# Kernel optimization log

Measured on AMD Instinct MI355X. Metric: run time of the kernel, lower is better.

## Reference

```python
import jax, jax.numpy as jnp
import numpy as np

NEG_INF = -1e9


def setup_inputs() -> dict:
    key = jax.random.key(0)
    ks = jax.random.split(key, 8)
    B, S, D = 8, 2048, 1024
    scale = 1.0 / np.sqrt(D)
    src = jax.random.normal(ks[0], (B, S, D), dtype=jnp.float32)
    pad_len = jax.random.randint(ks[1], (B,), 0, S // 10)
    pos = jnp.arange(S)[None, :]
    src_padding_mask = jnp.where(pos >= (S - pad_len)[:, None], NEG_INF, 0.0).astype(jnp.float32)[:, :, None]
    # causal (subsequent) additive mask [S,S]
    src_subsq_mask = jnp.where(jnp.triu(jnp.ones((S, S), dtype=bool), k=1), NEG_INF, 0.0).astype(jnp.float32)
    Wk = jax.random.normal(ks[2], (D, D), dtype=jnp.float32) * scale
    Wv = jax.random.normal(ks[3], (D, D), dtype=jnp.float32) * scale
    Wq = jax.random.normal(ks[4], (D, D), dtype=jnp.float32) * scale
    bk = jnp.zeros((D,), dtype=jnp.float32)
    bv = jnp.zeros((D,), dtype=jnp.float32)
    bq = jnp.zeros((D,), dtype=jnp.float32)
    return {"src": src, "src_padding_mask": src_padding_mask, "src_subsq_mask": src_subsq_mask,
            "Wk": Wk, "bk": bk, "Wv": Wv, "bv": bv, "Wq": Wq, "bq": bq}


def reference(src, src_padding_mask, src_subsq_mask, Wk, bk, Wv, bv, Wq, bq):
    d_model = src.shape[-1]
    # torch nn.Linear: x @ W.T + b
    keys = jnp.einsum('bsd,ed->bse', src, Wk) + bk
    values = jnp.einsum('bsd,ed->bse', src, Wv) + bv
    queries = jnp.einsum('bsd,ed->bse', src, Wq) + bq
    sqrt_d = jnp.asarray(d_model, src.dtype) ** 0.5
    att = jnp.einsum('bqd,bkd->bqk', queries, keys) / sqrt_d   # [B,S,S]
    att = att + jnp.swapaxes(src_padding_mask, 1, 2)           # [B,1,S] broadcast
    att = att + src_subsq_mask[None, :, :]                      # [1,S,S] broadcast
    att_softmax = jax.nn.softmax(att, axis=2)
    att_out = jnp.einsum('bqk,bkd->bqd', att_softmax, values)
    return att_out
```

## Files before the change

kernel.cpp:

```cpp
#include <hip/hip_runtime.h>
#include <cstdint>
#include <cstddef>

#define BATCH 8
#define SEQ   2048
#define DM    1024

typedef _Float16 half8 __attribute__((ext_vector_type(8)));
typedef _Float16 half4v __attribute__((ext_vector_type(4)));
typedef float floatx4 __attribute__((ext_vector_type(4)));
typedef float float4v __attribute__((ext_vector_type(4)));

#define GLOBAL_AS __attribute__((address_space(1)))
#define LDS_AS    __attribute__((address_space(3)))

__device__ __forceinline__ void gl_lds16(const _Float16* g, _Float16* l) {
    __builtin_amdgcn_global_load_lds((const GLOBAL_AS void*)g, (LDS_AS void*)l, 16, 0, 0);
}

__device__ __forceinline__ void gemm_bt_tile(
    const _Float16* __restrict__ A, const _Float16* __restrict__ B,
    int lda, int ldb, int kmax,
    _Float16* As, _Float16* Bs, floatx4 (&acc)[4][4])
{
    const int t = threadIdx.x;
    const int wave = t >> 6, lane = t & 63;
    const int l15 = lane & 15, kq = lane >> 4;
    const int wm = (wave >> 1) * 64, wn = (wave & 1) * 64;
    const int srow = wave * 8 + (lane >> 3);
    const int schunk = lane & 7;
    _Float16* AsW = As + wave * 512;
    _Float16* BsW = Bs + wave * 512;
    const int cslot = ((kq ^ (l15 & 7)) * 8);
    const int cslot1 = (((4 + kq) ^ (l15 & 7)) * 8);

    for (int k0 = 0; k0 < kmax; k0 += 64) {
        __syncthreads();
        #pragma unroll
        for (int i = 0; i < 4; i++) {
            const int r = srow + i * 32;
            const int gcol = (schunk ^ (r & 7)) * 8;
            gl_lds16(A + (size_t)r * lda + k0 + gcol, AsW + i * 2048);
            gl_lds16(B + (size_t)r * ldb + k0 + gcol, BsW + i * 2048);
        }
        __syncthreads();

        {
            half8 af[4], bfr[4];
            #pragma unroll
            for (int i = 0; i < 4; i++)
                af[i] = *(const half8*)&As[(wm + i * 16 + l15) * 64 + cslot];
            #pragma unroll
            for (int j = 0; j < 4; j++)
                bfr[j] = *(const half8*)&Bs[(wn + j * 16 + l15) * 64 + cslot];
            #pragma unroll
            for (int i = 0; i < 4; i++)
                #pragma unroll
                for (int j = 0; j < 4; j++)
                    acc[i][j] = __builtin_amdgcn_mfma_f32_16x16x32_f16(af[i], bfr[j], acc[i][j], 0, 0, 0);
        }
        {
            half8 af[4], bfr[4];
            #pragma unroll
            for (int i = 0; i < 4; i++)
                af[i] = *(const half8*)&As[(wm + i * 16 + l15) * 64 + cslot1];
            #pragma unroll
            for (int j = 0; j < 4; j++)
                bfr[j] = *(const half8*)&Bs[(wn + j * 16 + l15) * 64 + cslot1];
            #pragma unroll
            for (int i = 0; i < 4; i++)
                #pragma unroll
                for (int j = 0; j < 4; j++)
                    acc[i][j] = __builtin_amdgcn_mfma_f32_16x16x32_f16(af[i], bfr[j], acc[i][j], 0, 0, 0);
        }
    }
}

__global__ __launch_bounds__(256) void convert_inputs(
    const float* __restrict__ src,
    const float* __restrict__ Wk, const float* __restrict__ Wv, const float* __restrict__ Wq,
    _Float16* __restrict__ Xh, _Float16* __restrict__ Wh)
{
    const int gid = blockIdx.x * 256 + threadIdx.x;
    const int gs  = gridDim.x * 256;
    const int nX4 = BATCH * SEQ * DM / 4;
    const int nW4 = DM * DM / 4;
    const float4v* s4  = (const float4v*)src;
    const float4v* wk4 = (const float4v*)Wk;
    const float4v* wv4 = (const float4v*)Wv;
    const float4v* wq4 = (const float4v*)Wq;
    half4v* x4 = (half4v*)Xh;
    half4v* w4 = (half4v*)Wh;
    for (int i = gid; i < nX4; i += gs) {
        float4v v = s4[i];
        half4v h;
        #pragma unroll
        for (int e = 0; e < 4; e++) h[e] = (_Float16)v[e];
        x4[i] = h;
    }
    for (int i = gid; i < nW4; i += gs) {
        float4v a = wk4[i], b = wv4[i], c = wq4[i];
        half4v ha, hb, hc;
        #pragma unroll
        for (int e = 0; e < 4; e++) { ha[e] = (_Float16)a[e]; hb[e] = (_Float16)b[e]; hc[e] = (_Float16)c[e]; }
        w4[i]           = ha;
        w4[nW4 + i]     = hb;
        w4[2 * nW4 + i] = hc;
    }
}

__global__ __launch_bounds__(256) void qkv_gemm(
    const _Float16* __restrict__ Xh, const _Float16* __restrict__ Wh,
    const float* __restrict__ bk, const float* __restrict__ bv, const float* __restrict__ bq,
    _Float16* __restrict__ Kh, _Float16* __restrict__ Vt, _Float16* __restrict__ Qh)
{
    __shared__ __align__(16) _Float16 As[128 * 64];
    __shared__ __align__(16) _Float16 Bs[128 * 64];
    const int L = blockIdx.x;
    const int x = L & 7, s = L >> 3;
    const int z = s >> 7;
    const int r = s & 127;
    const int by = x * 16 + (r >> 3);
    const int bx = r & 7;

    const _Float16 *A, *B;
    if (z == 1) {
        A = Wh + (size_t)DM * DM + (size_t)bx * 128 * DM;
        B = Xh + (size_t)by * 128 * DM;
    } else {
        A = Xh + (size_t)by * 128 * DM;
        B = Wh + (z == 0 ? (size_t)0 : (size_t)2 * DM * DM) + (size_t)bx * 128 * DM;
    }
    floatx4 acc[4][4] = {};
    gemm_bt_tile(A, B, DM, DM, DM, As, Bs, acc);

    const int lane = threadIdx.x & 63, wave = threadIdx.x >> 6;
    const int l15 = lane & 15, kq = lane >> 4;
    const int wm = (wave >> 1) * 64, wn = (wave & 1) * 64;
    if (z == 1) {
        const int b = by >> 4, st = by & 15;
        #pragma unroll
        for (int i = 0; i < 4; i++)
            #pragma unroll
            for (int j = 0; j < 4; j++)
                #pragma unroll
                for (int rr = 0; rr < 4; rr++) {
                    int d = bx * 128 + wm + i * 16 + kq * 4 + rr;
                    int sIdx = st * 128 + wn + j * 16 + l15;
                    Vt[((size_t)b * DM + d) * SEQ + sIdx] = (_Float16)(acc[i][j][rr] + bv[d]);
                }
    } else {
        const float* bias = (z == 0) ? bk : bq;
        _Float16* outp    = (z == 0) ? Kh : Qh;
        #pragma unroll
        for (int i = 0; i < 4; i++)
            #pragma unroll
            for (int j = 0; j < 4; j++)
                #pragma unroll
                for (int rr = 0; rr < 4; rr++) {
                    int row = by * 128 + wm + i * 16 + kq * 4 + rr;
                    int col = bx * 128 + wn + j * 16 + l15;
                    outp[(size_t)row * DM + col] = (_Float16)(acc[i][j][rr] + bias[col]);
                }
    }
}

__global__ __launch_bounds__(256) void scores_gemm(
    const _Float16* __restrict__ Qh, const _Float16* __restrict__ Kh,
    const float* __restrict__ pad, _Float16* __restrict__ Sc)
{
    __shared__ __align__(16) _Float16 As[128 * 64];
    __shared__ __align__(16) _Float16 Bs[128 * 64];
    const int L = blockIdx.x;
    const int x = L & 7, s = L >> 3;
    const int b = s / 17, w = s % 17;
    int by, bx;
    if (w < 16 - x) { by = 15 - x; bx = w; }
    else            { by = x;      bx = w - (16 - x); }

    const _Float16* A = Qh + ((size_t)b * SEQ + by * 128) * DM;
    const _Float16* B = Kh + ((size_t)b * SEQ + bx * 128) * DM;
    floatx4 acc[4][4] = {};
    gemm_bt_tile(A, B, DM, DM, DM, As, Bs, acc);

    const int lane = threadIdx.x & 63, wave = threadIdx.x >> 6;
    const int l15 = lane & 15, kq = lane >> 4;
    const int wm = (wave >> 1) * 64, wn = (wave & 1) * 64;
    #pragma unroll
    for (int i = 0; i < 4; i++)
        #pragma unroll
        for (int j = 0; j < 4; j++)
            #pragma unroll
            for (int r = 0; r < 4; r++) {
                int row = by * 128 + wm + i * 16 + kq * 4 + r;
                int col = bx * 128 + wn + j * 16 + l15;
                Sc[((size_t)b * SEQ + row) * SEQ + col] =
                    (_Float16)(acc[i][j][r] * 0.03125f + pad[b * SEQ + col]);
            }
}

__global__ __launch_bounds__(256) void softmax_rows(_Float16* __restrict__ Sc)
{
    const int bid = blockIdx.x;
    const int b = bid >> 11, q = bid & (SEQ - 1);
    _Float16* row = Sc + ((size_t)b * SEQ + q) * SEQ;
    const int n = q + 1;
    const int kmaxr = ((q >> 7) + 1) << 7;
    const int t = threadIdx.x;
    const int c0 = t * 8;
    const bool active = (c0 < kmaxr);
    __shared__ float red[4];

    half8 v = {};
    if (active) v = *(const half8*)(row + c0);
    float f[8];
    float m = -3.0e38f;
    #pragma unroll
    for (int e = 0; e < 8; e++) {
        f[e] = (active && (c0 + e < n)) ? (float)v[e] : -3.0e38f;
        m = fmaxf(m, f[e]);
    }
    #pragma unroll
    for (int o = 32; o > 0; o >>= 1) m = fmaxf(m, __shfl_down(m, o));
    if ((t & 63) == 0) red[t >> 6] = m;
    __syncthreads();
    m = fmaxf(fmaxf(red[0], red[1]), fmaxf(red[2], red[3]));

    float ex[8], s = 0.f;
    #pragma unroll
    for (int e = 0; e < 8; e++) {
        ex[e] = (f[e] > -1.0e38f) ? __expf(f[e] - m) : 0.f;
        s += ex[e];
    }
    #pragma unroll
    for (int o = 32; o > 0; o >>= 1) s += __shfl_down(s, o);
    __syncthreads();
    if ((t & 63) == 0) red[t >> 6] = s;
    __syncthreads();
    s = red[0] + red[1] + red[2] + red[3];

    if (active) {
        const float inv = 1.0f / s;
        half8 o8;
        #pragma unroll
        for (int e = 0; e < 8; e++) o8[e] = (_Float16)(ex[e] * inv);
        *(half8*)(row + c0) = o8;
    }
}

__global__ __launch_bounds__(256) void pv_gemm(
    const _Float16* __restrict__ P, const _Float16* __restrict__ Vt,
    float* __restrict__ out)
{
    __shared__ __align__(16) _Float16 As[128 * 64];
    __shared__ __align__(16) _Float16 Bs[128 * 64];
    const int L = blockIdx.x;
    const int x = L & 7, s = L >> 3;
    const int b = s >> 4;
    const int r = s & 15;
    const int by = (r < 8) ? (15 - x) : x;
    const int bx = r & 7;

    const _Float16* A = P  + ((size_t)b * SEQ + by * 128) * SEQ;
    const _Float16* B = Vt + ((size_t)b * DM  + bx * 128) * SEQ;
    const int kmax = (by + 1) * 128;
    floatx4 acc[4][4] = {};
    gemm_bt_tile(A, B, SEQ, SEQ, kmax, As, Bs, acc);

    const int lane = threadIdx.x & 63, wave = threadIdx.x >> 6;
    const int l15 = lane & 15, kq = lane >> 4;
    const int wm = (wave >> 1) * 64, wn = (wave & 1) * 64;
    #pragma unroll
    for (int i = 0; i < 4; i++)
        #pragma unroll
        for (int j = 0; j < 4; j++)
            #pragma unroll
            for (int rr = 0; rr < 4; rr++) {
                int row = by * 128 + wm + i * 16 + kq * 4 + rr;
                int col = bx * 128 + wn + j * 16 + l15;
                out[((size_t)b * SEQ + row) * DM + col] = acc[i][j][rr];
            }
}

extern "C" void kernel_launch(void* const* d_in, const int* in_sizes, int n_in,
                              void* d_out, int out_size, void* d_ws, size_t ws_size,
                              hipStream_t stream) {
    const float* src = (const float*)d_in[0];
    const float* pad = (const float*)d_in[1];
    const float* Wk = (const float*)d_in[3];
    const float* bk = (const float*)d_in[4];
    const float* Wv = (const float*)d_in[5];
    const float* bv = (const float*)d_in[6];
    const float* Wq = (const float*)d_in[7];
    const float* bq = (const float*)d_in[8];
    float* out = (float*)d_out;

    char* ws = (char*)d_ws;
    _Float16* Wh = (_Float16*)(ws);
    _Float16* Qh = (_Float16*)(ws + 6291456);
    _Float16* Kh = (_Float16*)(ws + 39845888);
    _Float16* Vt = (_Float16*)(ws + 73400320);
    _Float16* Sc = (_Float16*)(ws + 106954752);
    _Float16* Xh = (_Float16*)d_out;

    convert_inputs<<<2048, 256, 0, stream>>>(src, Wk, Wv, Wq, Xh, Wh);
    qkv_gemm<<<3072, 256, 0, stream>>>(Xh, Wh, bk, bv, bq, Kh, Vt, Qh);
    scores_gemm<<<1088, 256, 0, stream>>>(Qh, Kh, pad, Sc);
    softmax_rows<<<BATCH * SEQ, 256, 0, stream>>>(Sc);
    pv_gemm<<<1024, 256, 0, stream>>>(Sc, Vt, out);
}
```

Before: 410.4 us.

## Switch GEMMs to 256x256 tiles with double-buffered 8-phase LDS pipeline

Replaces the 128x128 single-buffered GEMM tile with a 256x256 tile run by 512 threads. LDS is double-buffered and global-to-LDS loads are interleaved with MFMA phases, using explicit barriers, waitcnt and setprio. This targets exposed load latency and low reuse per byte, and launches fewer, larger blocks for the QKV, scores and PV stages. Causal tiling coarsens to 256, so more masked work is computed and softmax scans wider rows. The larger LDS footprint and register count may reduce occupancy.

```diff
diff --git a/kernel.cpp b/kernel.cpp
--- a/kernel.cpp
+++ b/kernel.cpp
@@ -18,61 +18,124 @@
     __builtin_amdgcn_global_load_lds((const GLOBAL_AS void*)g, (LDS_AS void*)l, 16, 0, 0);
 }
 
-__device__ __forceinline__ void gemm_bt_tile(
+__device__ __forceinline__ void stage128(const _Float16* __restrict__ g, int ld, int k0,
+                                         _Float16* l, int wave, int lane) {
+    const int rw = wave * 8 + (lane >> 3);
+    const int sl = lane & 7;
+    #pragma unroll
+    for (int i = 0; i < 2; i++) {
+        const int r = i * 64 + rw;
+        gl_lds16(g + (size_t)r * ld + k0 + ((sl ^ (r & 7)) << 3),
+                 l + ((i * 64 + wave * 8) << 6));
+    }
+}
+
+#define LDA4(BUF, HALFOFF)                                                    \
+    _Pragma("unroll")                                                         \
+    for (int i = 0; i < 4; i++) {                                             \
+        a[i][0] = *(const half8*)&SA[BUF][aoff + (HALFOFF) + i * 1024 + sl0]; \
+        a[i][1] = *(const half8*)&SA[BUF][aoff + (HALFOFF) + i * 1024 + sl1]; \
+    }
+#define LDB2(DST, BUF, HALFOFF)                                               \
+    _Pragma("unroll")                                                         \
+    for (int j = 0; j < 2; j++) {                                             \
+        DST[j][0] = *(const half8*)&SB[BUF][boff + (HALFOFF) + j * 4096 + sl0]; \
+        DST[j][1] = *(const half8*)&SB[BUF][boff + (HALFOFF) + j * 4096 + sl1]; \
+    }
+
+#define PH_MFMA(IOFF, JOFF, BREG)                                             \
+    __builtin_amdgcn_s_barrier();                                             \
+    asm volatile("s_waitcnt lgkmcnt(0)" ::: "memory");                        \
+    __builtin_amdgcn_s_setprio(1);                                            \
+    _Pragma("unroll")                                                         \
+    for (int i = 0; i < 4; i++) {                                             \
+        _Pragma("unroll")                                                     \
+        for (int j = 0; j < 2; j++) {                                         \
+            acc[(IOFF) + i][(JOFF) + j] = __builtin_amdgcn_mfma_f32_16x16x32_f16( \
+                a[i][0], BREG[j][0], acc[(IOFF) + i][(JOFF) + j], 0, 0, 0);   \
+            acc[(IOFF) + i][(JOFF) + j] = __builtin_amdgcn_mfma_f32_16x16x32_f16( \
+                a[i][1], BREG[j][1], acc[(IOFF) + i][(JOFF) + j], 0, 0, 0);   \
+        }                                                                     \
+    }                                                                         \
+    __builtin_amdgcn_s_setprio(0);
+
+__device__ __forceinline__ void gemm256_8ph(
     const _Float16* __restrict__ A, const _Float16* __restrict__ B,
-    int lda, int ldb, int kmax,
-    _Float16* As, _Float16* Bs, floatx4 (&acc)[4][4])
+    int lda, int ldb, int nkt,
+    _Float16 (&SA)[2][16384], _Float16 (&SB)[2][16384],
+    floatx4 (&acc)[8][4])
 {
     const int t = threadIdx.x;
     const int wave = t >> 6, lane = t & 63;
     const int l15 = lane & 15, kq = lane >> 4;
-    const int wm = (wave >> 1) * 64, wn = (wave & 1) * 64;
-    const int srow = wave * 8 + (lane >> 3);
-    const int schunk = lane & 7;
-    _Float16* AsW = As + wave * 512;
-    _Float16* BsW = Bs + wave * 512;
-    const int cslot = ((kq ^ (l15 & 7)) * 8);
-    const int cslot1 = (((4 + kq) ^ (l15 & 7)) * 8);
-
-    for (int k0 = 0; k0 < kmax; k0 += 64) {
-        __syncthreads();
-        #pragma unroll
-        for (int i = 0; i < 4; i++) {
-            const int r = srow + i * 32;
-            const int gcol = (schunk ^ (r & 7)) * 8;
-            gl_lds16(A + (size_t)r * lda + k0 + gcol, AsW + i * 2048);
-            gl_lds16(B + (size_t)r * ldb + k0 + gcol, BsW + i * 2048);
-        }
-        __syncthreads();
-
-        {
-            half8 af[4], bfr[4];
-            #pragma unroll
-            for (int i = 0; i < 4; i++)
-                af[i] = *(const half8*)&As[(wm + i * 16 + l15) * 64 + cslot];
-            #pragma unroll
-            for (int j = 0; j < 4; j++)
-                bfr[j] = *(const half8*)&Bs[(wn + j * 16 + l15) * 64 + cslot];
-            #pragma unroll
-            for (int i = 0; i < 4; i++)
-                #pragma unroll
-                for (int j = 0; j < 4; j++)
-                    acc[i][j] = __builtin_amdgcn_mfma_f32_16x16x32_f16(af[i], bfr[j], acc[i][j], 0, 0, 0);
-        }
-        {
-            half8 af[4], bfr[4];
-            #pragma unroll
-            for (int i = 0; i < 4; i++)
-                af[i] = *(const half8*)&As[(wm + i * 16 + l15) * 64 + cslot1];
-            #pragma unroll
-            for (int j = 0; j < 4; j++)
-                bfr[j] = *(const half8*)&Bs[(wn + j * 16 + l15) * 64 + cslot1];
-            #pragma unroll
-            for (int i = 0; i < 4; i++)
-                #pragma unroll
-                for (int j = 0; j < 4; j++)
-                    acc[i][j] = __builtin_amdgcn_mfma_f32_16x16x32_f16(af[i], bfr[j], acc[i][j], 0, 0, 0);
-        }
+    const int wm = wave >> 2, wn = wave & 3;
+
+    const int aoff = (wm * 64 + l15) << 6;
+    const int boff = (wn * 16 + l15) << 6;
+    const int sl0 = ((kq ^ (l15 & 7)) << 3);
+    const int sl1 = (((4 + kq) ^ (l15 & 7)) << 3);
+
+    const _Float16* A128 = A + (size_t)128 * lda;
+    const _Float16* B128 = B + (size_t)128 * ldb;
+
+    stage128(A,    lda, 0,  &SA[0][0],    wave, lane);
+    stage128(B,    ldb, 0,  &SB[0][0],    wave, lane);
+    stage128(A128, lda, 0,  &SA[0][8192], wave, lane);
+    stage128(B128, ldb, 0,  &SB[0][8192], wave, lane);
+    stage128(A,    lda, 64, &SA[1][0],    wave, lane);
+    stage128(B,    ldb, 64, &SB[1][0],    wave, lane);
+    asm volatile("s_waitcnt vmcnt(4)" ::: "memory");
+    __builtin_amdgcn_s_barrier();
+    __builtin_amdgcn_sched_barrier(0);
+
+    half8 a[4][2], b0[2][2], b1[2][2];
+
+    for (int kt = 0; kt < nkt; kt += 2) {
+        const bool more = (kt + 2) < nkt;
+        const int kA = (kt + 1) * 64, kB = (kt + 2) * 64, kC = (kt + 3) * 64;
+
+        LDA4(0, 0); LDB2(b0, 0, 0);
+        stage128(A128, lda, kA, &SA[1][8192], wave, lane);
+        PH_MFMA(0, 0, b0);
+        __builtin_amdgcn_s_barrier();
+
+        LDB2(b1, 0, 8192);
+        stage128(B128, ldb, kA, &SB[1][8192], wave, lane);
+        PH_MFMA(0, 2, b1);
+        __builtin_amdgcn_s_barrier();
+
+        LDA4(0, 8192);
+        if (more) stage128(A, lda, kB, &SA[0][0], wave, lane);
+        PH_MFMA(4, 0, b0);
+        __builtin_amdgcn_s_barrier();
+
+        if (more) stage128(B, ldb, kB, &SB[0][0], wave, lane);
+        PH_MFMA(4, 2, b1);
+        if (more) { asm volatile("s_waitcnt vmcnt(4)" ::: "memory"); }
+        else      { asm volatile("s_waitcnt vmcnt(0)" ::: "memory"); }
+        __builtin_amdgcn_s_barrier();
+        __builtin_amdgcn_sched_barrier(0);
+
+        LDA4(1, 0); LDB2(b0, 1, 0);
+        if (more) stage128(A128, lda, kB, &SA[0][8192], wave, lane);
+        PH_MFMA(0, 0, b0);
+        __builtin_amdgcn_s_barrier();
+
+        LDB2(b1, 1, 8192);
+        if (more) stage128(B128, ldb, kB, &SB[0][8192], wave, lane);
+        PH_MFMA(0, 2, b1);
+        __builtin_amdgcn_s_barrier();
+
+        LDA4(1, 8192);
+        if (more) stage128(A, lda, kC, &SA[1][0], wave, lane);
+        PH_MFMA(4, 0, b0);
+        __builtin_amdgcn_s_barrier();
+
+        if (more) stage128(B, ldb, kC, &SB[1][0], wave, lane);
+        PH_MFMA(4, 2, b1);
+        if (more) { asm volatile("s_waitcnt vmcnt(4)" ::: "memory"); }
+        __builtin_amdgcn_s_barrier();
+        __builtin_amdgcn_sched_barrier(0);
     }
 }
 
@@ -109,93 +172,94 @@
     }
 }
 
-__global__ __launch_bounds__(256) void qkv_gemm(
+__global__ __launch_bounds__(512, 2) void qkv_gemm(
     const _Float16* __restrict__ Xh, const _Float16* __restrict__ Wh,
     const float* __restrict__ bk, const float* __restrict__ bv, const float* __restrict__ bq,
     _Float16* __restrict__ Kh, _Float16* __restrict__ Vt, _Float16* __restrict__ Qh)
 {
-    __shared__ __align__(16) _Float16 As[128 * 64];
-    __shared__ __align__(16) _Float16 Bs[128 * 64];
+    __shared__ __align__(16) _Float16 SA[2][16384];
+    __shared__ __align__(16) _Float16 SB[2][16384];
     const int L = blockIdx.x;
-    const int x = L & 7, s = L >> 3;
-    const int z = s >> 7;
-    const int r = s & 127;
-    const int by = x * 16 + (r >> 3);
-    const int bx = r & 7;
-
+    const int lid = (L & 7) * 96 + (L >> 3);
+    const int z = lid >> 8;
+    const int r = lid & 255;
+    int by, bx;
     const _Float16 *A, *B;
     if (z == 1) {
-        A = Wh + (size_t)DM * DM + (size_t)bx * 128 * DM;
-        B = Xh + (size_t)by * 128 * DM;
+        by = r & 3; bx = r >> 2;
+        A = Wh + (size_t)DM * DM + (size_t)by * 256 * DM;
+        B = Xh + (size_t)bx * 256 * DM;
     } else {
-        A = Xh + (size_t)by * 128 * DM;
-        B = Wh + (z == 0 ? (size_t)0 : (size_t)2 * DM * DM) + (size_t)bx * 128 * DM;
-    }
-    floatx4 acc[4][4] = {};
-    gemm_bt_tile(A, B, DM, DM, DM, As, Bs, acc);
-
-    const int lane = threadIdx.x & 63, wave = threadIdx.x >> 6;
+        by = r >> 2; bx = r & 3;
+        A = Xh + (size_t)by * 256 * DM;
+        B = Wh + (z ? (size_t)2 * DM * DM : (size_t)0) + (size_t)bx * 256 * DM;
+    }
+    floatx4 acc[8][4] = {};
+    gemm256_8ph(A, B, DM, DM, 16, SA, SB, acc);
+
+    const int t = threadIdx.x, wave = t >> 6, lane = t & 63;
     const int l15 = lane & 15, kq = lane >> 4;
-    const int wm = (wave >> 1) * 64, wn = (wave & 1) * 64;
+    const int wm = wave >> 2, wn = wave & 3;
     if (z == 1) {
-        const int b = by >> 4, st = by & 15;
-        #pragma unroll
-        for (int i = 0; i < 4; i++)
+        #pragma unroll
+        for (int i = 0; i < 8; i++)
             #pragma unroll
             for (int j = 0; j < 4; j++)
                 #pragma unroll
                 for (int rr = 0; rr < 4; rr++) {
-                    int d = bx * 128 + wm + i * 16 + kq * 4 + rr;
-                    int sIdx = st * 128 + wn + j * 16 + l15;
-                    Vt[((size_t)b * DM + d) * SEQ + sIdx] = (_Float16)(acc[i][j][rr] + bv[d]);
+                    const int d  = by * 256 + wm * 64 + (i & 3) * 16 + (i >> 2) * 128 + kq * 4 + rr;
+                    const int sg = bx * 256 + wn * 16 + j * 64 + l15;
+                    const int b = sg >> 11, s = sg & (SEQ - 1);
+                    Vt[((size_t)b * DM + d) * SEQ + s] = (_Float16)(acc[i][j][rr] + bv[d]);
                 }
     } else {
-        const float* bias = (z == 0) ? bk : bq;
-        _Float16* outp    = (z == 0) ? Kh : Qh;
-        #pragma unroll
-        for (int i = 0; i < 4; i++)
+        const float* bias = z ? bq : bk;
+        _Float16* outp    = z ? Qh : Kh;
+        #pragma unroll
+        for (int i = 0; i < 8; i++)
             #pragma unroll
             for (int j = 0; j < 4; j++)
                 #pragma unroll
                 for (int rr = 0; rr < 4; rr++) {
-                    int row = by * 128 + wm + i * 16 + kq * 4 + rr;
-                    int col = bx * 128 + wn + j * 16 + l15;
+                    const int row = by * 256 + wm * 64 + (i & 3) * 16 + (i >> 2) * 128 + kq * 4 + rr;
+                    const int col = bx * 256 + wn * 16 + j * 64 + l15;
                     outp[(size_t)row * DM + col] = (_Float16)(acc[i][j][rr] + bias[col]);
                 }
     }
 }
 
-__global__ __launch_bounds__(256) void scores_gemm(
+__global__ __launch_bounds__(512, 2) void scores_gemm(
     const _Float16* __restrict__ Qh, const _Float16* __restrict__ Kh,
     const float* __restrict__ pad, _Float16* __restrict__ Sc)
 {
-    __shared__ __align__(16) _Float16 As[128 * 64];
-    __shared__ __align__(16) _Float16 Bs[128 * 64];
+    __shared__ __align__(16) _Float16 SA[2][16384];
+    __shared__ __align__(16) _Float16 SB[2][16384];
     const int L = blockIdx.x;
-    const int x = L & 7, s = L >> 3;
-    const int b = s / 17, w = s % 17;
-    int by, bx;
-    if (w < 16 - x) { by = 15 - x; bx = w; }
-    else            { by = x;      bx = w - (16 - x); }
-
-    const _Float16* A = Qh + ((size_t)b * SEQ + by * 128) * DM;
-    const _Float16* B = Kh + ((size_t)b * SEQ + bx * 128) * DM;
-    floatx4 acc[4][4] = {};
-    gemm_bt_tile(A, B, DM, DM, DM, As, Bs, acc);
-
-    const int lane = threadIdx.x & 63, wave = threadIdx.x >> 6;
+    const int lid = (L & 7) * 36 + (L >> 3);
+    const int b = lid / 36, tri = lid - b * 36;
+    int by = 0;
+    #pragma unroll
+    for (int u = 1; u <= 7; u++) if (tri >= (u * (u + 1)) / 2) by = u;
+    const int bx = tri - (by * (by + 1)) / 2;
+
+    const _Float16* A = Qh + ((size_t)b * SEQ + by * 256) * DM;
+    const _Float16* B = Kh + ((size_t)b * SEQ + bx * 256) * DM;
+    floatx4 acc[8][4] = {};
+    gemm256_8ph(A, B, DM, DM, 16, SA, SB, acc);
+
+    const int t = threadIdx.x, wave = t >> 6, lane = t & 63;
     const int l15 = lane & 15, kq = lane >> 4;
-    const int wm = (wave >> 1) * 64, wn = (wave & 1) * 64;
-    #pragma unroll
-    for (int i = 0; i < 4; i++)
+    const int wm = wave >> 2, wn = wave & 3;
+    #pragma unroll
+    for (int i = 0; i < 8; i++)
         #pragma unroll
         for (int j = 0; j < 4; j++)
             #pragma unroll
-            for (int r = 0; r < 4; r++) {
-                int row = by * 128 + wm + i * 16 + kq * 4 + r;
-                int col = bx * 128 + wn + j * 16 + l15;
+            for (int rr = 0; rr < 4; rr++) {
+                const int row = by * 256 + wm * 64 + (i & 3) * 16 + (i >> 2) * 128 + kq * 4 + rr;
+                const int col = bx * 256 + wn * 16 + j * 64 + l15;
                 Sc[((size_t)b * SEQ + row) * SEQ + col] =
-                    (_Float16)(acc[i][j][r] * 0.03125f + pad[b * SEQ + col]);
+                    (_Float16)(acc[i][j][rr] * 0.03125f + pad[b * SEQ + col]);
             }
 }
 
@@ -205,7 +269,7 @@
     const int b = bid >> 11, q = bid & (SEQ - 1);
     _Float16* row = Sc + ((size_t)b * SEQ + q) * SEQ;
     const int n = q + 1;
-    const int kmaxr = ((q >> 7) + 1) << 7;
+    const int kmaxr = ((q >> 8) + 1) << 8;
     const int t = threadIdx.x;
     const int c0 = t * 8;
     const bool active = (c0 < kmaxr);
@@ -248,36 +312,35 @@
     }
 }
 
-__global__ __launch_bounds__(256) void pv_gemm(
+__global__ __launch_bounds__(512, 2) void pv_gemm(
     const _Float16* __restrict__ P, const _Float16* __restrict__ Vt,
     float* __restrict__ out)
 {
-    __shared__ __align__(16) _Float16 As[128 * 64];
-    __shared__ __align__(16) _Float16 Bs[128 * 64];
+    __shared__ __align__(16) _Float16 SA[2][16384];
+    __shared__ __align__(16) _Float16 SB[2][16384];
     const int L = blockIdx.x;
-    const int x = L & 7, s = L >> 3;
-    const int b = s >> 4;
-    const int r = s & 15;
-    const int by = (r < 8) ? (15 - x) : x;
-    const int bx = r & 7;
-
-    const _Float16* A = P  + ((size_t)b * SEQ + by * 128) * SEQ;
-    const _Float16* B = Vt + ((size_t)b * DM  + bx * 128) * SEQ;
-    const int kmax = (by + 1) * 128;
-    floatx4 acc[4][4] = {};
-    gemm_bt_tile(A, B, SEQ, SEQ, kmax, As, Bs, acc);
-
-    const int lane = threadIdx.x & 63, wave = threadIdx.x >> 6;
+    const int lid = (L & 7) * 32 + (L >> 3);
+    const int b = lid >> 5, r = lid & 31;
+    const int by = 7 - (r >> 2);
+    const int bx = r & 3;
+
+    const _Float16* A = P  + ((size_t)b * SEQ + by * 256) * SEQ;
+    const _Float16* B = Vt + ((size_t)b * DM  + bx * 256) * SEQ;
+    const int nkt = (by + 1) * 4;
+    floatx4 acc[8][4] = {};
+    gemm256_8ph(A, B, SEQ, SEQ, nkt, SA, SB, acc);
+
+    const int t = threadIdx.x, wave = t >> 6, lane = t & 63;
     const int l15 = lane & 15, kq = lane >> 4;
-    const int wm = (wave >> 1) * 64, wn = (wave & 1) * 64;
-    #pragma unroll
-    for (int i = 0; i < 4; i++)
+    const int wm = wave >> 2, wn = wave & 3;
+    #pragma unroll
+    for (int i = 0; i < 8; i++)
         #pragma unroll
         for (int j = 0; j < 4; j++)
             #pragma unroll
             for (int rr = 0; rr < 4; rr++) {
-                int row = by * 128 + wm + i * 16 + kq * 4 + rr;
-                int col = bx * 128 + wn + j * 16 + l15;
+                const int row = by * 256 + wm * 64 + (i & 3) * 16 + (i >> 2) * 128 + kq * 4 + rr;
+                const int col = bx * 256 + wn * 16 + j * 64 + l15;
                 out[((size_t)b * SEQ + row) * DM + col] = acc[i][j][rr];
             }
 }
@@ -304,8 +367,8 @@
     _Float16* Xh = (_Float16*)d_out;
 
     convert_inputs<<<2048, 256, 0, stream>>>(src, Wk, Wv, Wq, Xh, Wh);
-    qkv_gemm<<<3072, 256, 0, stream>>>(Xh, Wh, bk, bv, bq, Kh, Vt, Qh);
-    scores_gemm<<<1088, 256, 0, stream>>>(Qh, Kh, pad, Sc);
+    qkv_gemm<<<768, 512, 0, stream>>>(Xh, Wh, bk, bv, bq, Kh, Vt, Qh);
+    scores_gemm<<<288, 512, 0, stream>>>(Qh, Kh, pad, Sc);
     softmax_rows<<<BATCH * SEQ, 256, 0, stream>>>(Sc);
-    pv_gemm<<<1024, 256, 0, stream>>>(Sc, Vt, out);
-}
+    pv_gemm<<<256, 512, 0, stream>>>(Sc, Vt, out);
+}
```

Result: faster. 384.5 us (-6.3%).
